# Performance work log

Measured on AMD Instinct MI355X. Metric: run time of the kernel, lower is better.

## Reference

```python
import jax, jax.numpy as jnp
import numpy as np

B, S, D, H = 2, 2048, 1024, 16
HD = D // H  # 64
EPS = 1e-8


def setup_inputs() -> dict:
    key = jax.random.key(0)
    ks = jax.random.split(key, 9)
    hidden_states = jax.random.normal(ks[0], (B, S, D), dtype=jnp.float32)
    # rotary tables: standard RoPE angles over half the head dim
    pos = jnp.arange(S, dtype=jnp.float32)[:, None]
    inv_freq = 1.0 / (10000.0 ** (jnp.arange(0, HD, 2, dtype=jnp.float32) / HD))  # [HD/2]
    ang = pos * inv_freq[None, :]  # [S, HD/2]
    sin = jnp.sin(ang)[None, None]  # [1,1,S,HD/2]
    cos = jnp.cos(ang)[None, None]
    s = 1.0 / np.sqrt(D)
    wq = jax.random.normal(ks[1], (D, D), dtype=jnp.float32) * s
    wk = jax.random.normal(ks[2], (D, D), dtype=jnp.float32) * s
    wv = jax.random.normal(ks[3], (D, D), dtype=jnp.float32) * s
    wo = jax.random.normal(ks[4], (D, D), dtype=jnp.float32) * s
    bo = jnp.zeros((D,), dtype=jnp.float32)
    scale = jnp.ones((D,), dtype=jnp.float32)
    return {"hidden_states": hidden_states, "sin": sin, "cos": cos,
            "wq": wq, "wk": wk, "wv": wv, "wo": wo, "bo": bo, "scale": scale}


def _heads(x):
    # [B,S,D] -> [B,H,S,HD]
    return x.reshape(B, S, H, HD).transpose(0, 2, 1, 3)


def _rotary(x, sin, cos):
    # interleaved RoPE: even/odd pairs
    x1, x2 = x[..., 0::2], x[..., 1::2]
    out = jnp.stack([x1 * cos - x2 * sin, x2 * cos + x1 * sin], axis=-1)
    return out.reshape(x.shape)


def reference(hidden_states, sin, cos, wq, wk, wv, wo, bo, scale):
    q = _rotary(_heads(hidden_states @ wq.T), sin, cos)
    k = _rotary(_heads(hidden_states @ wk.T), sin, cos)
    v = _rotary(_heads(hidden_states @ wv.T), sin, cos)
    scores = jnp.einsum("bhqd,bhkd->bhqk", q, k) / np.sqrt(HD)
    probs = jax.nn.softmax(scores, axis=-1)
    ctx = jnp.einsum("bhqk,bhkd->bhqd", probs, v)
    ctx = ctx.transpose(0, 2, 1, 3).reshape(B, S, D)
    out = ctx @ wo.T + bo
    x = out + hidden_states
    # RMSNorm: x / (||x||/sqrt(d) + eps) * scale
    rms = jnp.linalg.norm(x, axis=-1, keepdims=True) / np.sqrt(D)
    return scale * (x / (rms + EPS))
```

## Files before the change

kernel.cpp:

```cpp
#include <hip/hip_runtime.h>
#include <cmath>

#define BB 2
#define SS 2048
#define DD 1024
#define HH 16
#define HDIM 64
#define KDIM 1024
#define EPSF 1e-8f
#define QSCALE 0.18033688f

typedef __attribute__((ext_vector_type(8))) short bf16x8;
typedef __attribute__((ext_vector_type(4))) float f32x4;
typedef __attribute__((ext_vector_type(16))) float f32x16;

__device__ __forceinline__ ushort f2bf(float x) {
    unsigned u = __builtin_bit_cast(unsigned, x);
    u += 0x7FFFu + ((u >> 16) & 1u);
    return (ushort)(u >> 16);
}

__device__ __forceinline__ unsigned pack_bf16_trunc(float a, float b) {
    return __builtin_amdgcn_perm(__builtin_bit_cast(unsigned, b),
                                 __builtin_bit_cast(unsigned, a), 0x07060302u);
}

__device__ __forceinline__ float exp2_fast(float x) {
    float r;
    asm("v_exp_f32 %0, %1" : "=v"(r) : "v"(x));
    return r;
}

__device__ __forceinline__ void gload_lds16(const ushort* g, ushort* l) {
    __builtin_amdgcn_global_load_lds(
        (const __attribute__((address_space(1))) unsigned*)g,
        (__attribute__((address_space(3))) unsigned*)l, 16, 0, 0);
}

__global__ __launch_bounds__(256) void conv_all(
    const float* __restrict__ hs, const float* __restrict__ wq,
    const float* __restrict__ wk, const float* __restrict__ wv,
    const float* __restrict__ wo, ushort* __restrict__ dst)
{
    const int i = blockIdx.x * 256 + threadIdx.x;
    const int HS4 = (BB * SS * DD) / 4;
    const int W4 = (DD * DD) / 4;
    const float* src;
    int off;
    if (i < HS4) { src = hs; off = i; }
    else {
        const int j = i - HS4;
        const int seg = j / W4;
        off = j - seg * W4;
        src = (seg == 0) ? wq : (seg == 1) ? wk : (seg == 2) ? wv : wo;
    }
    const float4 v = ((const float4*)src)[off];
    ushort4 o;
    o.x = f2bf(v.x); o.y = f2bf(v.y); o.z = f2bf(v.z); o.w = f2bf(v.w);
    ((ushort4*)dst)[i] = o;
}

__global__ __launch_bounds__(256) void gemm_qkv_mfma(
    const ushort* __restrict__ A,
    const ushort* __restrict__ Wq, const ushort* __restrict__ Wk,
    const ushort* __restrict__ Wv,
    const float* __restrict__ sinp, const float* __restrict__ cosp,
    ushort* __restrict__ Qb, ushort* __restrict__ Kb, ushort* __restrict__ Vtb)
{
    const int cb = blockIdx.y;
    const int z = cb >> 3;
    const int col0 = (cb & 7) * 128;
    const ushort* W = (z == 0) ? Wq : (z == 1) ? Wk : Wv;
    ushort* O = (z == 0) ? Qb : (z == 1) ? Kb : Vtb;
    const int row0 = blockIdx.x * 128;
    const float qs = (z == 0) ? QSCALE : 1.0f;

    __shared__ __align__(16) ushort As[128 * 32];
    __shared__ __align__(16) ushort Bs[128 * 32];

    const int tid = threadIdx.x;
    const int w = tid >> 6, lane = tid & 63;
    const int quad = lane >> 4, l15 = lane & 15;
    const int m_off = (w >> 1) * 64, n_off = (w & 1) * 64;

    f32x4 acc[4][4] = {};

    for (int k0 = 0; k0 < KDIM; k0 += 32) {
#pragma unroll
        for (int it = 0; it < 2; ++it) {
            const int L = (it * 4 + w) * 64 + lane;
            const int r = L >> 2, c8 = (L & 3) * 8;
            gload_lds16(A + (size_t)(row0 + r) * KDIM + k0 + c8, &As[L * 8]);
            gload_lds16(W + (size_t)(col0 + r) * KDIM + k0 + c8, &Bs[L * 8]);
        }
        __syncthreads();
        bf16x8 af[4], bfr[4];
#pragma unroll
        for (int i = 0; i < 4; ++i) {
            af[i]  = *(const bf16x8*)&As[(m_off + i * 16 + l15) * 32 + quad * 8];
            bfr[i] = *(const bf16x8*)&Bs[(n_off + i * 16 + l15) * 32 + quad * 8];
        }
#pragma unroll
        for (int i = 0; i < 4; ++i)
#pragma unroll
            for (int j = 0; j < 4; ++j)
                acc[i][j] = __builtin_amdgcn_mfma_f32_16x16x32_bf16(
                    af[i], bfr[j], acc[i][j], 0, 0, 0);
        __syncthreads();
    }

    const int b = (row0 + m_off) / SS;
#pragma unroll
    for (int mi = 0; mi < 4; ++mi) {
        const int mrow = row0 + m_off + mi * 16 + quad * 4;
#pragma unroll
        for (int ni = 0; ni < 4; ++ni) {
            const int c = col0 + n_off + ni * 16 + l15;
            const int h = c >> 6, e = c & 63;
            const int bh = b * HH + h;
            float outv[4];
#pragma unroll
            for (int r = 0; r < 4; ++r) {
                const int s = (mrow + r) & (SS - 1);
                const float sv = sinp[s * (HDIM / 2) + (e >> 1)];
                const float cv = cosp[s * (HDIM / 2) + (e >> 1)];
                const float v = acc[mi][ni][r];
                const float vp = __shfl_xor(v, 1);
                outv[r] = ((l15 & 1) ? (v * cv + vp * sv) : (v * cv - vp * sv)) * qs;
            }
            if (z < 2) {
#pragma unroll
                for (int r = 0; r < 4; ++r) {
                    const int s = (mrow + r) & (SS - 1);
                    const ushort mine = f2bf(outv[r]);
                    const ushort part = (ushort)__shfl_xor((int)mine, 1);
                    if (!(l15 & 1))
                        *(unsigned*)(O + ((size_t)(bh * SS + s)) * HDIM + e) =
                            (unsigned)mine | ((unsigned)part << 16);
                }
            } else {
                ushort4 pk;
                pk.x = f2bf(outv[0]); pk.y = f2bf(outv[1]);
                pk.z = f2bf(outv[2]); pk.w = f2bf(outv[3]);
                const int s0 = mrow & (SS - 1);
                *(ushort4*)(O + ((size_t)(bh * HDIM + e)) * SS + s0) = pk;
            }
        }
    }
}

__global__ __launch_bounds__(256, 2) void attn_mfma(
    const ushort* __restrict__ Qb, const ushort* __restrict__ Kb,
    const ushort* __restrict__ Vtb, ushort* __restrict__ ctx)
{
    const int wg  = blockIdx.x;
    const int lin = (wg & 7) * 64 + (wg >> 3);
    const int bh   = lin >> 4;
    const int qblk = lin & 15;
    const int b = bh / HH, h = bh % HH;
    const int q0 = qblk * 128;
    const int tid = threadIdx.x;
    const int w = tid >> 6;
    const int lane = tid & 63;
    const int l31 = lane & 31;
    const int g = lane >> 5;
    const int strip = w >> 1;
    const int phase = w & 1;

    __shared__ __align__(16) ushort kvb[2][2][2][64][32];

    const ushort* Qh = Qb  + (size_t)bh * SS * HDIM;
    const ushort* Kh = Kb  + (size_t)bh * SS * HDIM;
    const ushort* Vh = Vtb + (size_t)bh * HDIM * SS;

    const int qrowA = q0 + strip * 64 + l31;
    const int qrowB = qrowA + 32;
    bf16x8 qf[2][4];
#pragma unroll
    for (int ks = 0; ks < 4; ++ks) {
        qf[0][ks] = *(const bf16x8*)(Qh + (size_t)qrowA * HDIM + ks * 16 + g * 8);
        qf[1][ks] = *(const bf16x8*)(Qh + (size_t)qrowB * HDIM + ks * 16 + g * 8);
    }

    f32x16 cacc[2][2] = {};
    float ls0a = 0.f, ls0b = 0.f, ls1a = 0.f, ls1b = 0.f;

    const int lr = lane >> 2;
    const int c16 = lane & 3;
    const int lc = c16 * 8;
    const int swc = (c16 ^ ((lr >> 1) & 3)) * 8;
    const int srow = w * 16 + lr;
    const int rsw = (l31 >> 1) & 3;

    uint4 rk0, rk1, rv0, rv1;

#define LOAD_STAGE(K0)                                                        \
    do {                                                                      \
        const ushort* Kp = Kh + (size_t)((K0) + srow) * HDIM + lc;            \
        const ushort* Vp = Vh + (size_t)srow * SS + (K0) + lc;                \
        rk0 = *(const uint4*)(Kp);                                            \
        rk1 = *(const uint4*)(Kp + 32);                                       \
        rv0 = *(const uint4*)(Vp);                                            \
        rv1 = *(const uint4*)(Vp + 32);                                       \
    } while (0)

#define WRITE_STAGE(bufi)                                                     \
    do {                                                                      \
        *(uint4*)&kvb[bufi][0][0][srow][swc] = rk0;                           \
        *(uint4*)&kvb[bufi][0][1][srow][swc] = rk1;                           \
        *(uint4*)&kvb[bufi][1][0][srow][swc] = rv0;                           \
        *(uint4*)&kvb[bufi][1][1][srow][swc] = rv1;                           \
    } while (0)

    const int NT = SS / 64;

    LOAD_STAGE(0);
    WRITE_STAGE(0);
    LOAD_STAGE(64);

    for (int t = 0; t < NT; ++t) {
        __syncthreads();
        const int cur = t & 1;

        bf16x8 kf[4];
#pragma unroll
        for (int ks = 0; ks < 4; ++ks)
            kf[ks] = *(const bf16x8*)&kvb[cur][0][ks >> 1]
                [phase * 32 + l31][(((ks & 1) * 2 + g) ^ rsw) * 8];

        if (t + 1 < NT) WRITE_STAGE(cur ^ 1);
        if (t + 2 < NT) LOAD_STAGE((t + 2) * 64);

        f32x16 sacc0 = {}, sacc1 = {};
        __builtin_amdgcn_s_setprio(1);
#pragma unroll
        for (int ks = 0; ks < 4; ++ks) {
            sacc0 = __builtin_amdgcn_mfma_f32_32x32x16_bf16(
                kf[ks], qf[0][ks], sacc0, 0, 0, 0);
            sacc1 = __builtin_amdgcn_mfma_f32_32x32x16_bf16(
                kf[ks], qf[1][ks], sacc1, 0, 0, 0);
        }
        __builtin_amdgcn_s_setprio(0);

        unsigned pk[2][8];
#pragma unroll
        for (int i = 0; i < 8; ++i) {
            const float pa0 = exp2_fast(sacc0[2 * i]);
            const float pb0 = exp2_fast(sacc0[2 * i + 1]);
            const float pa1 = exp2_fast(sacc1[2 * i]);
            const float pb1 = exp2_fast(sacc1[2 * i + 1]);
            if (i & 1) { ls0b += pa0 + pb0; ls1b += pa1 + pb1; }
            else       { ls0a += pa0 + pb0; ls1a += pa1 + pb1; }
            pk[0][i] = pack_bf16_trunc(pa0, pb0);
            pk[1][i] = pack_bf16_trunc(pa1, pb1);
        }

#pragma unroll
        for (int ks = 0; ks < 2; ++ks) {
            const int bq = ks * 4;
            unsigned a00 = pk[0][bq + 0], a01 = pk[0][bq + 1];
            unsigned b00 = pk[0][bq + 2], b01 = pk[0][bq + 3];
            unsigned a10 = pk[1][bq + 0], a11 = pk[1][bq + 1];
            unsigned b10 = pk[1][bq + 2], b11 = pk[1][bq + 3];
            asm("v_permlane32_swap_b32 %0, %1" : "+v"(a00), "+v"(b00));
            asm("v_permlane32_swap_b32 %0, %1" : "+v"(a01), "+v"(b01));
            asm("v_permlane32_swap_b32 %0, %1" : "+v"(a10), "+v"(b10));
            asm("v_permlane32_swap_b32 %0, %1" : "+v"(a11), "+v"(b11));
            union { unsigned u[4]; bf16x8 v; } pf0, pf1;
            pf0.u[0] = a00; pf0.u[1] = a01; pf0.u[2] = b00; pf0.u[3] = b01;
            pf1.u[0] = a10; pf1.u[1] = a11; pf1.u[2] = b10; pf1.u[3] = b11;
            __builtin_amdgcn_s_setprio(1);
#pragma unroll
            for (int dt = 0; dt < 2; ++dt) {
                const bf16x8 vf = *(const bf16x8*)&kvb[cur][1][phase]
                    [dt * 32 + l31][((ks * 2 + g) ^ rsw) * 8];
                cacc[0][dt] = __builtin_amdgcn_mfma_f32_32x32x16_bf16(
                    vf, pf0.v, cacc[0][dt], 0, 0, 0);
                cacc[1][dt] = __builtin_amdgcn_mfma_f32_32x32x16_bf16(
                    vf, pf1.v, cacc[1][dt], 0, 0, 0);
            }
            __builtin_amdgcn_s_setprio(0);
        }
    }

    float lsq[2];
    lsq[0] = ls0a + ls0b;
    lsq[1] = ls1a + ls1b;
    lsq[0] += __shfl_xor(lsq[0], 32);
    lsq[1] += __shfl_xor(lsq[1], 32);

    float* mlds = (float*)kvb;
    const int mbase = strip * 2112 + lane * 33;
#pragma unroll
    for (int qs = 0; qs < 2; ++qs) {
        __syncthreads();
        if (phase == 1) {
#pragma unroll
            for (int dt = 0; dt < 2; ++dt)
#pragma unroll
                for (int i = 0; i < 16; ++i)
                    mlds[mbase + dt * 16 + i] = cacc[qs][dt][i];
            mlds[mbase + 32] = lsq[qs];
        }
        __syncthreads();
        if (phase == 0) {
            f32x16 cf[2];
#pragma unroll
            for (int dt = 0; dt < 2; ++dt)
#pragma unroll
                for (int i = 0; i < 16; ++i)
                    cf[dt][i] = cacc[qs][dt][i] + mlds[mbase + dt * 16 + i];
            const float inv = 1.f / (lsq[qs] + mlds[mbase + 32]);

            const int qrow = (qs == 0) ? qrowA : qrowB;
            const size_t obase = ((size_t)(b * SS + qrow)) * DD + h * HDIM;
#pragma unroll
            for (int dt = 0; dt < 2; ++dt)
#pragma unroll
                for (int tt = 0; tt < 4; ++tt) {
                    ushort4 o;
                    o.x = f2bf(cf[dt][tt * 4 + 0] * inv);
                    o.y = f2bf(cf[dt][tt * 4 + 1] * inv);
                    o.z = f2bf(cf[dt][tt * 4 + 2] * inv);
                    o.w = f2bf(cf[dt][tt * 4 + 3] * inv);
                    *(ushort4*)(ctx + obase + dt * 32 + tt * 8 + g * 4) = o;
                }
        }
    }
#undef LOAD_STAGE
#undef WRITE_STAGE
}

__global__ __launch_bounds__(256) void gemm_out_mfma(
    const ushort* __restrict__ A, const ushort* __restrict__ W,
    const float* __restrict__ bias, float* __restrict__ Out)
{
    const int row0 = blockIdx.x * 128;
    const int col0 = blockIdx.y * 64;

    __shared__ __align__(16) ushort As[128 * 32];
    __shared__ __align__(16) ushort Bs[64 * 32];

    const int tid = threadIdx.x;
    const int w = tid >> 6, lane = tid & 63;
    const int quad = lane >> 4, l15 = lane & 15;
    const int m_off = (w >> 1) * 64, n_off = (w & 1) * 32;

    f32x4 acc[4][2] = {};

    for (int k0 = 0; k0 < KDIM; k0 += 32) {
#pragma unroll
        for (int it = 0; it < 2; ++it) {
            const int L = (it * 4 + w) * 64 + lane;
            const int r = L >> 2, c8 = (L & 3) * 8;
            gload_lds16(A + (size_t)(row0 + r) * KDIM + k0 + c8, &As[L * 8]);
        }
        {
            const int L = w * 64 + lane;
            const int r = L >> 2, c8 = (L & 3) * 8;
            gload_lds16(W + (size_t)(col0 + r) * KDIM + k0 + c8, &Bs[L * 8]);
        }
        __syncthreads();
        bf16x8 af[4], bfr[2];
#pragma unroll
        for (int i = 0; i < 4; ++i)
            af[i] = *(const bf16x8*)&As[(m_off + i * 16 + l15) * 32 + quad * 8];
#pragma unroll
        for (int j = 0; j < 2; ++j)
            bfr[j] = *(const bf16x8*)&Bs[(n_off + j * 16 + l15) * 32 + quad * 8];
#pragma unroll
        for (int i = 0; i < 4; ++i)
#pragma unroll
            for (int j = 0; j < 2; ++j)
                acc[i][j] = __builtin_amdgcn_mfma_f32_16x16x32_bf16(
                    af[i], bfr[j], acc[i][j], 0, 0, 0);
        __syncthreads();
    }

#pragma unroll
    for (int mi = 0; mi < 4; ++mi) {
        const int mrow = row0 + m_off + mi * 16 + quad * 4;
#pragma unroll
        for (int ni = 0; ni < 2; ++ni) {
            const int c = col0 + n_off + ni * 16 + l15;
            const float bv = bias[c];
#pragma unroll
            for (int r = 0; r < 4; ++r)
                Out[(size_t)(mrow + r) * DD + c] = acc[mi][ni][r] + bv;
        }
    }
}

__global__ __launch_bounds__(256) void resid_rmsnorm(
    const float* __restrict__ proj, const float* __restrict__ hs,
    const float* __restrict__ scale, float* __restrict__ out)
{
    const int t = blockIdx.x;
    const int tid = threadIdx.x;
    const size_t base = (size_t)t * DD + tid * 4;

    const float4 p4 = *(const float4*)(proj + base);
    const float4 h4 = *(const float4*)(hs + base);
    float x0 = p4.x + h4.x, x1 = p4.y + h4.y, x2 = p4.z + h4.z, x3 = p4.w + h4.w;
    float ss = x0 * x0 + x1 * x1 + x2 * x2 + x3 * x3;

#pragma unroll
    for (int off = 1; off < 64; off <<= 1) ss += __shfl_xor(ss, off);

    __shared__ float wsum[4];
    if ((tid & 63) == 0) wsum[tid >> 6] = ss;
    __syncthreads();
    const float total = wsum[0] + wsum[1] + wsum[2] + wsum[3];
    const float inv = 1.f / (sqrtf(total * (1.f / DD)) + EPSF);

    const float4 s4 = *(const float4*)(scale + tid * 4);
    float4 o;
    o.x = s4.x * x0 * inv;
    o.y = s4.y * x1 * inv;
    o.z = s4.z * x2 * inv;
    o.w = s4.w * x3 * inv;
    *(float4*)(out + base) = o;
}

extern "C" void kernel_launch(void* const* d_in, const int* in_sizes, int n_in,
                              void* d_out, int out_size, void* d_ws, size_t ws_size,
                              hipStream_t stream) {
    const float* hs    = (const float*)d_in[0];
    const float* sinp  = (const float*)d_in[1];
    const float* cosp  = (const float*)d_in[2];
    const float* wq    = (const float*)d_in[3];
    const float* wk    = (const float*)d_in[4];
    const float* wv    = (const float*)d_in[5];
    const float* wo    = (const float*)d_in[6];
    const float* bo    = (const float*)d_in[7];
    const float* scale = (const float*)d_in[8];
    float* out = (float*)d_out;

    unsigned char* wsb = (unsigned char*)d_ws;
    const size_t MAT = (size_t)BB * SS * DD;
    const size_t WN  = (size_t)DD * DD;
    ushort* Abf = (ushort*)wsb;
    ushort* Wqb = Abf + MAT;
    ushort* Wkb = Wqb + WN;
    ushort* Wvb = Wkb + WN;
    ushort* Wob = Wvb + WN;
    ushort* Qb  = Wob + WN;
    ushort* Kb  = Qb + MAT;
    ushort* Vtb = Kb + MAT;
    ushort* ctxb = Vtb + MAT;
    float* proj = (float*)(ctxb + MAT);

    const int nconv4 = (int)((MAT + 4 * WN) / 4);
    conv_all<<<dim3(nconv4 / 256), 256, 0, stream>>>(hs, wq, wk, wv, wo, Abf);

    gemm_qkv_mfma<<<dim3(32, 24), 256, 0, stream>>>(Abf, Wqb, Wkb, Wvb,
                                                    sinp, cosp, Qb, Kb, Vtb);
    attn_mfma<<<dim3(512), 256, 0, stream>>>(Qb, Kb, Vtb, ctxb);
    gemm_out_mfma<<<dim3(32, 16), 256, 0, stream>>>(ctxb, Wob, bo, proj);
    resid_rmsnorm<<<dim3(BB * SS), 256, 0, stream>>>(proj, hs, scale, out);
}
```

Before: 195.3 us.

## Split attention key range across four waves per query strip with 512-thread blocks

The attention kernel moves from 256 to 512 threads per block. Four waves now share each 64-row query strip, each taking a quarter of every 128-key tile, where before two waves each took half of a 64-key tile. The K/V shared-memory stage doubles to 128 keys with a reworked V layout, and the final reduction sums the partial contexts and row sums of three peer waves through LDS. This aims to hide latency with more waves per CU, at the cost of extra reduction traffic, a larger LDS footprint and tighter register limits from launch_bounds(512,4).

```diff
diff --git a/kernel.cpp b/kernel.cpp
--- a/kernel.cpp
+++ b/kernel.cpp
@@ -149,7 +149,7 @@
     }
 }
 
-__global__ __launch_bounds__(256, 2) void attn_mfma(
+__global__ __launch_bounds__(512, 4) void attn_mfma(
     const ushort* __restrict__ Qb, const ushort* __restrict__ Kb,
     const ushort* __restrict__ Vtb, ushort* __restrict__ ctx)
 {
@@ -164,10 +164,12 @@
     const int lane = tid & 63;
     const int l31 = lane & 31;
     const int g = lane >> 5;
-    const int strip = w >> 1;
-    const int phase = w & 1;
-
-    __shared__ __align__(16) ushort kvb[2][2][2][64][32];
+    const int strip = w >> 2;
+    const int phase = w & 3;
+
+    __shared__ __align__(16) ushort kvb[32768];
+#define KOFF(bf, hf, row) (((((bf) * 2 + (hf)) * 128) + (row)) * 32)
+#define VOFF(bf, kq, row) (16384 + ((((bf) * 4 + (kq)) * 64) + (row)) * 32)
 
     const ushort* Qh = Qb  + (size_t)bh * SS * HDIM;
     const ushort* Kh = Kb  + (size_t)bh * SS * HDIM;
@@ -190,6 +192,9 @@
     const int lc = c16 * 8;
     const int swc = (c16 ^ ((lr >> 1) & 3)) * 8;
     const int srow = w * 16 + lr;
+    const int vrow = (w & 3) * 16 + lr;
+    const int vkh  = (w >> 2) * 64;
+    const int kq0  = (w >> 2) * 2, kq1 = kq0 + 1;
     const int rsw = (l31 >> 1) & 3;
 
     uint4 rk0, rk1, rv0, rv1;
@@ -197,7 +202,7 @@
 #define LOAD_STAGE(K0)                                                        \
     do {                                                                      \
         const ushort* Kp = Kh + (size_t)((K0) + srow) * HDIM + lc;            \
-        const ushort* Vp = Vh + (size_t)srow * SS + (K0) + lc;                \
+        const ushort* Vp = Vh + (size_t)vrow * SS + (K0) + vkh + lc;          \
         rk0 = *(const uint4*)(Kp);                                            \
         rk1 = *(const uint4*)(Kp + 32);                                       \
         rv0 = *(const uint4*)(Vp);                                            \
@@ -206,17 +211,17 @@
 
 #define WRITE_STAGE(bufi)                                                     \
     do {                                                                      \
-        *(uint4*)&kvb[bufi][0][0][srow][swc] = rk0;                           \
-        *(uint4*)&kvb[bufi][0][1][srow][swc] = rk1;                           \
-        *(uint4*)&kvb[bufi][1][0][srow][swc] = rv0;                           \
-        *(uint4*)&kvb[bufi][1][1][srow][swc] = rv1;                           \
+        *(uint4*)&kvb[KOFF(bufi, 0, srow) + swc] = rk0;                       \
+        *(uint4*)&kvb[KOFF(bufi, 1, srow) + swc] = rk1;                       \
+        *(uint4*)&kvb[VOFF(bufi, kq0, vrow) + swc] = rv0;                     \
+        *(uint4*)&kvb[VOFF(bufi, kq1, vrow) + swc] = rv1;                     \
     } while (0)
 
-    const int NT = SS / 64;
+    const int NT = SS / 128;
 
     LOAD_STAGE(0);
     WRITE_STAGE(0);
-    LOAD_STAGE(64);
+    LOAD_STAGE(128);
 
     for (int t = 0; t < NT; ++t) {
         __syncthreads();
@@ -225,11 +230,11 @@
         bf16x8 kf[4];
 #pragma unroll
         for (int ks = 0; ks < 4; ++ks)
-            kf[ks] = *(const bf16x8*)&kvb[cur][0][ks >> 1]
-                [phase * 32 + l31][(((ks & 1) * 2 + g) ^ rsw) * 8];
+            kf[ks] = *(const bf16x8*)&kvb[KOFF(cur, ks >> 1, phase * 32 + l31)
+                                          + (((ks & 1) * 2 + g) ^ rsw) * 8];
 
         if (t + 1 < NT) WRITE_STAGE(cur ^ 1);
-        if (t + 2 < NT) LOAD_STAGE((t + 2) * 64);
+        if (t + 2 < NT) LOAD_STAGE((t + 2) * 128);
 
         f32x16 sacc0 = {}, sacc1 = {};
         __builtin_amdgcn_s_setprio(1);
@@ -272,8 +277,8 @@
             __builtin_amdgcn_s_setprio(1);
 #pragma unroll
             for (int dt = 0; dt < 2; ++dt) {
-                const bf16x8 vf = *(const bf16x8*)&kvb[cur][1][phase]
-                    [dt * 32 + l31][((ks * 2 + g) ^ rsw) * 8];
+                const bf16x8 vf = *(const bf16x8*)&kvb[VOFF(cur, phase, dt * 32 + l31)
+                                                       + ((ks * 2 + g) ^ rsw) * 8];
                 cacc[0][dt] = __builtin_amdgcn_mfma_f32_32x32x16_bf16(
                     vf, pf0.v, cacc[0][dt], 0, 0, 0);
                 cacc[1][dt] = __builtin_amdgcn_mfma_f32_32x32x16_bf16(
@@ -290,27 +295,37 @@
     lsq[1] += __shfl_xor(lsq[1], 32);
 
     float* mlds = (float*)kvb;
-    const int mbase = strip * 2112 + lane * 33;
+    const int wbase = ((strip * 3 + (phase - 1)) * 64 + lane) * 33;
 #pragma unroll
     for (int qs = 0; qs < 2; ++qs) {
         __syncthreads();
-        if (phase == 1) {
+        if (phase != 0) {
 #pragma unroll
             for (int dt = 0; dt < 2; ++dt)
 #pragma unroll
                 for (int i = 0; i < 16; ++i)
-                    mlds[mbase + dt * 16 + i] = cacc[qs][dt][i];
-            mlds[mbase + 32] = lsq[qs];
+                    mlds[wbase + dt * 16 + i] = cacc[qs][dt][i];
+            mlds[wbase + 32] = lsq[qs];
         }
         __syncthreads();
         if (phase == 0) {
             f32x16 cf[2];
+            float lt = lsq[qs];
 #pragma unroll
             for (int dt = 0; dt < 2; ++dt)
 #pragma unroll
-                for (int i = 0; i < 16; ++i)
-                    cf[dt][i] = cacc[qs][dt][i] + mlds[mbase + dt * 16 + i];
-            const float inv = 1.f / (lsq[qs] + mlds[mbase + 32]);
+                for (int i = 0; i < 16; ++i) cf[dt][i] = cacc[qs][dt][i];
+#pragma unroll
+            for (int p = 0; p < 3; ++p) {
+                const int rbase = ((strip * 3 + p) * 64 + lane) * 33;
+#pragma unroll
+                for (int dt = 0; dt < 2; ++dt)
+#pragma unroll
+                    for (int i = 0; i < 16; ++i)
+                        cf[dt][i] += mlds[rbase + dt * 16 + i];
+                lt += mlds[rbase + 32];
+            }
+            const float inv = 1.f / lt;
 
             const int qrow = (qs == 0) ? qrowA : qrowB;
             const size_t obase = ((size_t)(b * SS + qrow)) * DD + h * HDIM;
@@ -329,6 +344,8 @@
     }
 #undef LOAD_STAGE
 #undef WRITE_STAGE
+#undef KOFF
+#undef VOFF
 }
 
 __global__ __launch_bounds__(256) void gemm_out_mfma(
@@ -455,7 +472,7 @@
 
     gemm_qkv_mfma<<<dim3(32, 24), 256, 0, stream>>>(Abf, Wqb, Wkb, Wvb,
                                                     sinp, cosp, Qb, Kb, Vtb);
-    attn_mfma<<<dim3(512), 256, 0, stream>>>(Qb, Kb, Vtb, ctxb);
+    attn_mfma<<<dim3(512), 512, 0, stream>>>(Qb, Kb, Vtb, ctxb);
     gemm_out_mfma<<<dim3(32, 16), 256, 0, stream>>>(ctxb, Wob, bo, proj);
     resid_rmsnorm<<<dim3(BB * SS), 256, 0, stream>>>(proj, hs, scale, out);
 }
```

Measured after the change: 322.1 us. +65.0%, slower.

## Load K/V fragments directly from global into registers, dropping LDS staging

Applied to the files above, without the earlier changes.

The attention kernel stops staging K and V tiles through a double-buffered shared-memory ring with per-tile barriers. Each wave now loads its MFMA operand fragments straight from global memory into registers, with K prefetched one tile ahead via ping-pong register sets and the loop unrolled by two. This removes the LDS writes and reads and the __syncthreads per tile. In exchange, waves that share K/V no longer share one load, so global/L2 traffic rises and each global access exposes more latency. Register pressure also grows, which at launch bounds of 2 may cause spills.

```diff
diff --git a/kernel.cpp b/kernel.cpp
--- a/kernel.cpp
+++ b/kernel.cpp
@@ -167,7 +167,7 @@
     const int strip = w >> 1;
     const int phase = w & 1;
 
-    __shared__ __align__(16) ushort kvb[2][2][2][64][32];
+    __shared__ float mlds[2 * 64 * 33];
 
     const ushort* Qh = Qb  + (size_t)bh * SS * HDIM;
     const ushort* Kh = Kb  + (size_t)bh * SS * HDIM;
@@ -185,102 +185,93 @@
     f32x16 cacc[2][2] = {};
     float ls0a = 0.f, ls0b = 0.f, ls1a = 0.f, ls1b = 0.f;
 
-    const int lr = lane >> 2;
-    const int c16 = lane & 3;
-    const int lc = c16 * 8;
-    const int swc = (c16 ^ ((lr >> 1) & 3)) * 8;
-    const int srow = w * 16 + lr;
-    const int rsw = (l31 >> 1) & 3;
-
-    uint4 rk0, rk1, rv0, rv1;
-
-#define LOAD_STAGE(K0)                                                        \
+    const ushort* Kbase = Kh + (size_t)(phase * 32 + l31) * HDIM + g * 8;
+    const ushort* Vbase = Vh + (size_t)l31 * SS + phase * 32 + g * 8;
+
+    uint4 ka0, ka1, ka2, ka3;
+    uint4 kb0, kb1, kb2, kb3;
+    uint4 v00, v01, v10, v11;
+
+#define LOADK(p0, p1, p2, p3, T)                                              \
     do {                                                                      \
-        const ushort* Kp = Kh + (size_t)((K0) + srow) * HDIM + lc;            \
-        const ushort* Vp = Vh + (size_t)srow * SS + (K0) + lc;                \
-        rk0 = *(const uint4*)(Kp);                                            \
-        rk1 = *(const uint4*)(Kp + 32);                                       \
-        rv0 = *(const uint4*)(Vp);                                            \
-        rv1 = *(const uint4*)(Vp + 32);                                       \
+        const ushort* Kp_ = Kbase + (size_t)(T) * 64 * HDIM;                  \
+        p0 = *(const uint4*)(Kp_);                                            \
+        p1 = *(const uint4*)(Kp_ + 16);                                       \
+        p2 = *(const uint4*)(Kp_ + 32);                                       \
+        p3 = *(const uint4*)(Kp_ + 48);                                       \
     } while (0)
 
-#define WRITE_STAGE(bufi)                                                     \
+#define LOADV(T)                                                              \
     do {                                                                      \
-        *(uint4*)&kvb[bufi][0][0][srow][swc] = rk0;                           \
-        *(uint4*)&kvb[bufi][0][1][srow][swc] = rk1;                           \
-        *(uint4*)&kvb[bufi][1][0][srow][swc] = rv0;                           \
-        *(uint4*)&kvb[bufi][1][1][srow][swc] = rv1;                           \
+        const ushort* Vp_ = Vbase + (T) * 64;                                 \
+        v00 = *(const uint4*)(Vp_);                                           \
+        v01 = *(const uint4*)(Vp_ + 16);                                      \
+        v10 = *(const uint4*)(Vp_ + (size_t)32 * SS);                         \
+        v11 = *(const uint4*)(Vp_ + (size_t)32 * SS + 16);                    \
     } while (0)
 
+#define TILE(kc0, kc1, kc2, kc3, kn0, kn1, kn2, kn3, T, PF)                   \
+    do {                                                                      \
+        LOADV(T);                                                             \
+        if (PF) LOADK(kn0, kn1, kn2, kn3, (T) + 1);                           \
+        const bf16x8 kf0 = __builtin_bit_cast(bf16x8, kc0);                   \
+        const bf16x8 kf1 = __builtin_bit_cast(bf16x8, kc1);                   \
+        const bf16x8 kf2 = __builtin_bit_cast(bf16x8, kc2);                   \
+        const bf16x8 kf3 = __builtin_bit_cast(bf16x8, kc3);                   \
+        f32x16 sacc0 = {}, sacc1 = {};                                        \
+        __builtin_amdgcn_s_setprio(1);                                        \
+        sacc0 = __builtin_amdgcn_mfma_f32_32x32x16_bf16(kf0, qf[0][0], sacc0, 0, 0, 0); \
+        sacc1 = __builtin_amdgcn_mfma_f32_32x32x16_bf16(kf0, qf[1][0], sacc1, 0, 0, 0); \
+        sacc0 = __builtin_amdgcn_mfma_f32_32x32x16_bf16(kf1, qf[0][1], sacc0, 0, 0, 0); \
+        sacc1 = __builtin_amdgcn_mfma_f32_32x32x16_bf16(kf1, qf[1][1], sacc1, 0, 0, 0); \
+        sacc0 = __builtin_amdgcn_mfma_f32_32x32x16_bf16(kf2, qf[0][2], sacc0, 0, 0, 0); \
+        sacc1 = __builtin_amdgcn_mfma_f32_32x32x16_bf16(kf2, qf[1][2], sacc1, 0, 0, 0); \
+        sacc0 = __builtin_amdgcn_mfma_f32_32x32x16_bf16(kf3, qf[0][3], sacc0, 0, 0, 0); \
+        sacc1 = __builtin_amdgcn_mfma_f32_32x32x16_bf16(kf3, qf[1][3], sacc1, 0, 0, 0); \
+        __builtin_amdgcn_s_setprio(0);                                        \
+        unsigned pk[2][8];                                                    \
+        _Pragma("unroll")                                                     \
+        for (int i = 0; i < 8; ++i) {                                         \
+            const float pa0 = exp2_fast(sacc0[2 * i]);                        \
+            const float pb0 = exp2_fast(sacc0[2 * i + 1]);                    \
+            const float pa1 = exp2_fast(sacc1[2 * i]);                        \
+            const float pb1 = exp2_fast(sacc1[2 * i + 1]);                    \
+            if (i & 1) { ls0b += pa0 + pb0; ls1b += pa1 + pb1; }              \
+            else       { ls0a += pa0 + pb0; ls1a += pa1 + pb1; }              \
+            pk[0][i] = pack_bf16_trunc(pa0, pb0);                             \
+            pk[1][i] = pack_bf16_trunc(pa1, pb1);                             \
+        }                                                                     \
+        _Pragma("unroll")                                                     \
+        for (int ks = 0; ks < 2; ++ks) {                                      \
+            const int bq = ks * 4;                                            \
+            unsigned a00 = pk[0][bq + 0], a01 = pk[0][bq + 1];                \
+            unsigned b00 = pk[0][bq + 2], b01 = pk[0][bq + 3];                \
+            unsigned a10 = pk[1][bq + 0], a11 = pk[1][bq + 1];                \
+            unsigned b10 = pk[1][bq + 2], b11 = pk[1][bq + 3];                \
+            asm("v_permlane32_swap_b32 %0, %1" : "+v"(a00), "+v"(b00));       \
+            asm("v_permlane32_swap_b32 %0, %1" : "+v"(a01), "+v"(b01));       \
+            asm("v_permlane32_swap_b32 %0, %1" : "+v"(a10), "+v"(b10));       \
+            asm("v_permlane32_swap_b32 %0, %1" : "+v"(a11), "+v"(b11));       \
+            union { unsigned u[4]; bf16x8 v; } pf0, pf1;                      \
+            pf0.u[0] = a00; pf0.u[1] = a01; pf0.u[2] = b00; pf0.u[3] = b01;   \
+            pf1.u[0] = a10; pf1.u[1] = a11; pf1.u[2] = b10; pf1.u[3] = b11;   \
+            const bf16x8 vf0 = __builtin_bit_cast(bf16x8, ks ? v01 : v00);    \
+            const bf16x8 vf1 = __builtin_bit_cast(bf16x8, ks ? v11 : v10);    \
+            __builtin_amdgcn_s_setprio(1);                                    \
+            cacc[0][0] = __builtin_amdgcn_mfma_f32_32x32x16_bf16(vf0, pf0.v, cacc[0][0], 0, 0, 0); \
+            cacc[1][0] = __builtin_amdgcn_mfma_f32_32x32x16_bf16(vf0, pf1.v, cacc[1][0], 0, 0, 0); \
+            cacc[0][1] = __builtin_amdgcn_mfma_f32_32x32x16_bf16(vf1, pf0.v, cacc[0][1], 0, 0, 0); \
+            cacc[1][1] = __builtin_amdgcn_mfma_f32_32x32x16_bf16(vf1, pf1.v, cacc[1][1], 0, 0, 0); \
+            __builtin_amdgcn_s_setprio(0);                                    \
+        }                                                                     \
+    } while (0)
+
     const int NT = SS / 64;
 
-    LOAD_STAGE(0);
-    WRITE_STAGE(0);
-    LOAD_STAGE(64);
-
-    for (int t = 0; t < NT; ++t) {
-        __syncthreads();
-        const int cur = t & 1;
-
-        bf16x8 kf[4];
-#pragma unroll
-        for (int ks = 0; ks < 4; ++ks)
-            kf[ks] = *(const bf16x8*)&kvb[cur][0][ks >> 1]
-                [phase * 32 + l31][(((ks & 1) * 2 + g) ^ rsw) * 8];
-
-        if (t + 1 < NT) WRITE_STAGE(cur ^ 1);
-        if (t + 2 < NT) LOAD_STAGE((t + 2) * 64);
-
-        f32x16 sacc0 = {}, sacc1 = {};
-        __builtin_amdgcn_s_setprio(1);
-#pragma unroll
-        for (int ks = 0; ks < 4; ++ks) {
-            sacc0 = __builtin_amdgcn_mfma_f32_32x32x16_bf16(
-                kf[ks], qf[0][ks], sacc0, 0, 0, 0);
-            sacc1 = __builtin_amdgcn_mfma_f32_32x32x16_bf16(
-                kf[ks], qf[1][ks], sacc1, 0, 0, 0);
-        }
-        __builtin_amdgcn_s_setprio(0);
-
-        unsigned pk[2][8];
-#pragma unroll
-        for (int i = 0; i < 8; ++i) {
-            const float pa0 = exp2_fast(sacc0[2 * i]);
-            const float pb0 = exp2_fast(sacc0[2 * i + 1]);
-            const float pa1 = exp2_fast(sacc1[2 * i]);
-            const float pb1 = exp2_fast(sacc1[2 * i + 1]);
-            if (i & 1) { ls0b += pa0 + pb0; ls1b += pa1 + pb1; }
-            else       { ls0a += pa0 + pb0; ls1a += pa1 + pb1; }
-            pk[0][i] = pack_bf16_trunc(pa0, pb0);
-            pk[1][i] = pack_bf16_trunc(pa1, pb1);
-        }
-
-#pragma unroll
-        for (int ks = 0; ks < 2; ++ks) {
-            const int bq = ks * 4;
-            unsigned a00 = pk[0][bq + 0], a01 = pk[0][bq + 1];
-            unsigned b00 = pk[0][bq + 2], b01 = pk[0][bq + 3];
-            unsigned a10 = pk[1][bq + 0], a11 = pk[1][bq + 1];
-            unsigned b10 = pk[1][bq + 2], b11 = pk[1][bq + 3];
-            asm("v_permlane32_swap_b32 %0, %1" : "+v"(a00), "+v"(b00));
-            asm("v_permlane32_swap_b32 %0, %1" : "+v"(a01), "+v"(b01));
-            asm("v_permlane32_swap_b32 %0, %1" : "+v"(a10), "+v"(b10));
-            asm("v_permlane32_swap_b32 %0, %1" : "+v"(a11), "+v"(b11));
-            union { unsigned u[4]; bf16x8 v; } pf0, pf1;
-            pf0.u[0] = a00; pf0.u[1] = a01; pf0.u[2] = b00; pf0.u[3] = b01;
-            pf1.u[0] = a10; pf1.u[1] = a11; pf1.u[2] = b10; pf1.u[3] = b11;
-            __builtin_amdgcn_s_setprio(1);
-#pragma unroll
-            for (int dt = 0; dt < 2; ++dt) {
-                const bf16x8 vf = *(const bf16x8*)&kvb[cur][1][phase]
-                    [dt * 32 + l31][((ks * 2 + g) ^ rsw) * 8];
-                cacc[0][dt] = __builtin_amdgcn_mfma_f32_32x32x16_bf16(
-                    vf, pf0.v, cacc[0][dt], 0, 0, 0);
-                cacc[1][dt] = __builtin_amdgcn_mfma_f32_32x32x16_bf16(
-                    vf, pf1.v, cacc[1][dt], 0, 0, 0);
-            }
-            __builtin_amdgcn_s_setprio(0);
-        }
+    LOADK(ka0, ka1, ka2, ka3, 0);
+    for (int t = 0; t < NT; t += 2) {
+        TILE(ka0, ka1, ka2, ka3, kb0, kb1, kb2, kb3, t, 1);
+        TILE(kb0, kb1, kb2, kb3, ka0, ka1, ka2, ka3, t + 1, (t + 2 < NT));
     }
 
     float lsq[2];
@@ -289,7 +280,6 @@
     lsq[0] += __shfl_xor(lsq[0], 32);
     lsq[1] += __shfl_xor(lsq[1], 32);
 
-    float* mlds = (float*)kvb;
     const int mbase = strip * 2112 + lane * 33;
 #pragma unroll
     for (int qs = 0; qs < 2; ++qs) {
@@ -327,8 +317,9 @@
                 }
         }
     }
-#undef LOAD_STAGE
-#undef WRITE_STAGE
+#undef LOADK
+#undef LOADV
+#undef TILE
 }
 
 __global__ __launch_bounds__(256) void gemm_out_mfma(
```

Result: slower. 218.5 us (+11.9%).

## Double attention KV tile to 128 keys and remap GEMM workgroups per XCD

Applied to the files above, without the earlier changes.

The attention kernel now stages 128 keys per iteration instead of 64, halving the number of barrier/loop iterations and loading twice as much K/V per stage into a larger LDS buffer. This doubles the register staging and the LDS footprint (64KB), which may reduce occupancy below the two-blocks-per-CU launch bound. Separately, both projection GEMMs switch to a 1D grid with an XCD-aware block remapping so that neighbouring tiles share L2 on the same die.

```diff
diff --git a/kernel.cpp b/kernel.cpp
--- a/kernel.cpp
+++ b/kernel.cpp
@@ -67,12 +67,14 @@
     const float* __restrict__ sinp, const float* __restrict__ cosp,
     ushort* __restrict__ Qb, ushort* __restrict__ Kb, ushort* __restrict__ Vtb)
 {
-    const int cb = blockIdx.y;
+    const int wg = blockIdx.x;
+    const int lin = (wg & 7) * 96 + (wg >> 3);
+    const int cb = lin >> 5;
+    const int row0 = (lin & 31) * 128;
     const int z = cb >> 3;
     const int col0 = (cb & 7) * 128;
     const ushort* W = (z == 0) ? Wq : (z == 1) ? Wk : Wv;
     ushort* O = (z == 0) ? Qb : (z == 1) ? Kb : Vtb;
-    const int row0 = blockIdx.x * 128;
     const float qs = (z == 0) ? QSCALE : 1.0f;
 
     __shared__ __align__(16) ushort As[128 * 32];
@@ -167,7 +169,9 @@
     const int strip = w >> 1;
     const int phase = w & 1;
 
-    __shared__ __align__(16) ushort kvb[2][2][2][64][32];
+    __shared__ __align__(16) ushort kvb[32768];
+#define KOFF(bf, hf, row) (((((bf) * 2 + (hf)) * 128) + (row)) * 32)
+#define VOFF(bf, kq, row) (16384 + ((((bf) * 4 + (kq)) * 64) + (row)) * 32)
 
     const ushort* Qh = Qb  + (size_t)bh * SS * HDIM;
     const ushort* Kh = Kb  + (size_t)bh * SS * HDIM;
@@ -192,7 +196,7 @@
     const int srow = w * 16 + lr;
     const int rsw = (l31 >> 1) & 3;
 
-    uint4 rk0, rk1, rv0, rv1;
+    uint4 rk0, rk1, rk2, rk3, rv0, rv1, rv2, rv3;
 
 #define LOAD_STAGE(K0)                                                        \
     do {                                                                      \
@@ -200,86 +204,101 @@
         const ushort* Vp = Vh + (size_t)srow * SS + (K0) + lc;                \
         rk0 = *(const uint4*)(Kp);                                            \
         rk1 = *(const uint4*)(Kp + 32);                                       \
+        rk2 = *(const uint4*)(Kp + (size_t)64 * HDIM);                        \
+        rk3 = *(const uint4*)(Kp + (size_t)64 * HDIM + 32);                   \
         rv0 = *(const uint4*)(Vp);                                            \
         rv1 = *(const uint4*)(Vp + 32);                                       \
+        rv2 = *(const uint4*)(Vp + 64);                                       \
+        rv3 = *(const uint4*)(Vp + 96);                                       \
     } while (0)
 
 #define WRITE_STAGE(bufi)                                                     \
     do {                                                                      \
-        *(uint4*)&kvb[bufi][0][0][srow][swc] = rk0;                           \
-        *(uint4*)&kvb[bufi][0][1][srow][swc] = rk1;                           \
-        *(uint4*)&kvb[bufi][1][0][srow][swc] = rv0;                           \
-        *(uint4*)&kvb[bufi][1][1][srow][swc] = rv1;                           \
+        *(uint4*)&kvb[KOFF(bufi, 0, srow)      + swc] = rk0;                  \
+        *(uint4*)&kvb[KOFF(bufi, 1, srow)      + swc] = rk1;                  \
+        *(uint4*)&kvb[KOFF(bufi, 0, 64 + srow) + swc] = rk2;                  \
+        *(uint4*)&kvb[KOFF(bufi, 1, 64 + srow) + swc] = rk3;                  \
+        *(uint4*)&kvb[VOFF(bufi, 0, srow) + swc] = rv0;                       \
+        *(uint4*)&kvb[VOFF(bufi, 1, srow) + swc] = rv1;                       \
+        *(uint4*)&kvb[VOFF(bufi, 2, srow) + swc] = rv2;                       \
+        *(uint4*)&kvb[VOFF(bufi, 3, srow) + swc] = rv3;                       \
     } while (0)
 
-    const int NT = SS / 64;
+    const int NT = SS / 128;
 
     LOAD_STAGE(0);
     WRITE_STAGE(0);
-    LOAD_STAGE(64);
+    LOAD_STAGE(128);
 
     for (int t = 0; t < NT; ++t) {
         __syncthreads();
         const int cur = t & 1;
 
-        bf16x8 kf[4];
-#pragma unroll
-        for (int ks = 0; ks < 4; ++ks)
-            kf[ks] = *(const bf16x8*)&kvb[cur][0][ks >> 1]
-                [phase * 32 + l31][(((ks & 1) * 2 + g) ^ rsw) * 8];
-
-        if (t + 1 < NT) WRITE_STAGE(cur ^ 1);
-        if (t + 2 < NT) LOAD_STAGE((t + 2) * 64);
-
-        f32x16 sacc0 = {}, sacc1 = {};
-        __builtin_amdgcn_s_setprio(1);
-#pragma unroll
-        for (int ks = 0; ks < 4; ++ks) {
-            sacc0 = __builtin_amdgcn_mfma_f32_32x32x16_bf16(
-                kf[ks], qf[0][ks], sacc0, 0, 0, 0);
-            sacc1 = __builtin_amdgcn_mfma_f32_32x32x16_bf16(
-                kf[ks], qf[1][ks], sacc1, 0, 0, 0);
-        }
-        __builtin_amdgcn_s_setprio(0);
-
-        unsigned pk[2][8];
-#pragma unroll
-        for (int i = 0; i < 8; ++i) {
-            const float pa0 = exp2_fast(sacc0[2 * i]);
-            const float pb0 = exp2_fast(sacc0[2 * i + 1]);
-            const float pa1 = exp2_fast(sacc1[2 * i]);
-            const float pb1 = exp2_fast(sacc1[2 * i + 1]);
-            if (i & 1) { ls0b += pa0 + pb0; ls1b += pa1 + pb1; }
-            else       { ls0a += pa0 + pb0; ls1a += pa1 + pb1; }
-            pk[0][i] = pack_bf16_trunc(pa0, pb0);
-            pk[1][i] = pack_bf16_trunc(pa1, pb1);
-        }
-
-#pragma unroll
-        for (int ks = 0; ks < 2; ++ks) {
-            const int bq = ks * 4;
-            unsigned a00 = pk[0][bq + 0], a01 = pk[0][bq + 1];
-            unsigned b00 = pk[0][bq + 2], b01 = pk[0][bq + 3];
-            unsigned a10 = pk[1][bq + 0], a11 = pk[1][bq + 1];
-            unsigned b10 = pk[1][bq + 2], b11 = pk[1][bq + 3];
-            asm("v_permlane32_swap_b32 %0, %1" : "+v"(a00), "+v"(b00));
-            asm("v_permlane32_swap_b32 %0, %1" : "+v"(a01), "+v"(b01));
-            asm("v_permlane32_swap_b32 %0, %1" : "+v"(a10), "+v"(b10));
-            asm("v_permlane32_swap_b32 %0, %1" : "+v"(a11), "+v"(b11));
-            union { unsigned u[4]; bf16x8 v; } pf0, pf1;
-            pf0.u[0] = a00; pf0.u[1] = a01; pf0.u[2] = b00; pf0.u[3] = b01;
-            pf1.u[0] = a10; pf1.u[1] = a11; pf1.u[2] = b10; pf1.u[3] = b11;
+#pragma unroll
+        for (int u = 0; u < 2; ++u) {
+            bf16x8 kf[4];
+#pragma unroll
+            for (int ks = 0; ks < 4; ++ks)
+                kf[ks] = *(const bf16x8*)&kvb[
+                    KOFF(cur, ks >> 1, u * 64 + phase * 32 + l31)
+                    + (((ks & 1) * 2 + g) ^ rsw) * 8];
+
+            if (u == 0) {
+                if (t + 1 < NT) WRITE_STAGE(cur ^ 1);
+                if (t + 2 < NT) LOAD_STAGE((t + 2) * 128);
+            }
+
+            f32x16 sacc0 = {}, sacc1 = {};
             __builtin_amdgcn_s_setprio(1);
 #pragma unroll
-            for (int dt = 0; dt < 2; ++dt) {
-                const bf16x8 vf = *(const bf16x8*)&kvb[cur][1][phase]
-                    [dt * 32 + l31][((ks * 2 + g) ^ rsw) * 8];
-                cacc[0][dt] = __builtin_amdgcn_mfma_f32_32x32x16_bf16(
-                    vf, pf0.v, cacc[0][dt], 0, 0, 0);
-                cacc[1][dt] = __builtin_amdgcn_mfma_f32_32x32x16_bf16(
-                    vf, pf1.v, cacc[1][dt], 0, 0, 0);
+            for (int ks = 0; ks < 4; ++ks) {
+                sacc0 = __builtin_amdgcn_mfma_f32_32x32x16_bf16(
+                    kf[ks], qf[0][ks], sacc0, 0, 0, 0);
+                sacc1 = __builtin_amdgcn_mfma_f32_32x32x16_bf16(
+                    kf[ks], qf[1][ks], sacc1, 0, 0, 0);
             }
             __builtin_amdgcn_s_setprio(0);
+
+            unsigned pk[2][8];
+#pragma unroll
+            for (int i = 0; i < 8; ++i) {
+                const float pa0 = exp2_fast(sacc0[2 * i]);
+                const float pb0 = exp2_fast(sacc0[2 * i + 1]);
+                const float pa1 = exp2_fast(sacc1[2 * i]);
+                const float pb1 = exp2_fast(sacc1[2 * i + 1]);
+                if (i & 1) { ls0b += pa0 + pb0; ls1b += pa1 + pb1; }
+                else       { ls0a += pa0 + pb0; ls1a += pa1 + pb1; }
+                pk[0][i] = pack_bf16_trunc(pa0, pb0);
+                pk[1][i] = pack_bf16_trunc(pa1, pb1);
+            }
+
+#pragma unroll
+            for (int ks = 0; ks < 2; ++ks) {
+                const int bq = ks * 4;
+                unsigned a00 = pk[0][bq + 0], a01 = pk[0][bq + 1];
+                unsigned b00 = pk[0][bq + 2], b01 = pk[0][bq + 3];
+                unsigned a10 = pk[1][bq + 0], a11 = pk[1][bq + 1];
+                unsigned b10 = pk[1][bq + 2], b11 = pk[1][bq + 3];
+                asm("v_permlane32_swap_b32 %0, %1" : "+v"(a00), "+v"(b00));
+                asm("v_permlane32_swap_b32 %0, %1" : "+v"(a01), "+v"(b01));
+                asm("v_permlane32_swap_b32 %0, %1" : "+v"(a10), "+v"(b10));
+                asm("v_permlane32_swap_b32 %0, %1" : "+v"(a11), "+v"(b11));
+                union { unsigned u4[4]; bf16x8 v; } pf0, pf1;
+                pf0.u4[0] = a00; pf0.u4[1] = a01; pf0.u4[2] = b00; pf0.u4[3] = b01;
+                pf1.u4[0] = a10; pf1.u4[1] = a11; pf1.u4[2] = b10; pf1.u4[3] = b11;
+                __builtin_amdgcn_s_setprio(1);
+#pragma unroll
+                for (int dt = 0; dt < 2; ++dt) {
+                    const bf16x8 vf = *(const bf16x8*)&kvb[
+                        VOFF(cur, u * 2 + phase, dt * 32 + l31)
+                        + ((ks * 2 + g) ^ rsw) * 8];
+                    cacc[0][dt] = __builtin_amdgcn_mfma_f32_32x32x16_bf16(
+                        vf, pf0.v, cacc[0][dt], 0, 0, 0);
+                    cacc[1][dt] = __builtin_amdgcn_mfma_f32_32x32x16_bf16(
+                        vf, pf1.v, cacc[1][dt], 0, 0, 0);
+                }
+                __builtin_amdgcn_s_setprio(0);
+            }
         }
     }
 
@@ -329,14 +348,18 @@
     }
 #undef LOAD_STAGE
 #undef WRITE_STAGE
+#undef KOFF
+#undef VOFF
 }
 
 __global__ __launch_bounds__(256) void gemm_out_mfma(
     const ushort* __restrict__ A, const ushort* __restrict__ W,
     const float* __restrict__ bias, float* __restrict__ Out)
 {
-    const int row0 = blockIdx.x * 128;
-    const int col0 = blockIdx.y * 64;
+    const int wg = blockIdx.x;
+    const int lin = (wg & 7) * 64 + (wg >> 3);
+    const int row0 = (lin & 31) * 128;
+    const int col0 = (lin >> 5) * 64;
 
     __shared__ __align__(16) ushort As[128 * 32];
     __shared__ __align__(16) ushort Bs[64 * 32];
@@ -453,9 +476,9 @@
     const int nconv4 = (int)((MAT + 4 * WN) / 4);
     conv_all<<<dim3(nconv4 / 256), 256, 0, stream>>>(hs, wq, wk, wv, wo, Abf);
 
-    gemm_qkv_mfma<<<dim3(32, 24), 256, 0, stream>>>(Abf, Wqb, Wkb, Wvb,
-                                                    sinp, cosp, Qb, Kb, Vtb);
+    gemm_qkv_mfma<<<dim3(768), 256, 0, stream>>>(Abf, Wqb, Wkb, Wvb,
+                                                 sinp, cosp, Qb, Kb, Vtb);
     attn_mfma<<<dim3(512), 256, 0, stream>>>(Qb, Kb, Vtb, ctxb);
-    gemm_out_mfma<<<dim3(32, 16), 256, 0, stream>>>(ctxb, Wob, bo, proj);
+    gemm_out_mfma<<<dim3(512), 256, 0, stream>>>(ctxb, Wob, bo, proj);
     resid_rmsnorm<<<dim3(BB * SS), 256, 0, stream>>>(proj, hs, scale, out);
 }
```

Result: slower. 199.7 us (+2.3%).
